# Optimization experiments

Hardware: AMD Instinct MI355X
Metric: run time of the kernel (lower is better)

The kernel has to match this reference:

```python
import jax, jax.numpy as jnp
import numpy as np

B = 65536
IN_F = 1024
OUT_F = 1024


def setup_inputs() -> dict:
    key = jax.random.key(0)
    k1, k2 = jax.random.split(key)
    x = jax.random.normal(k1, (B, IN_F), dtype=jnp.float32)
    # init matches torch: normal(0, sqrt(2/(in+out)))
    std = np.sqrt(2.0 / (IN_F + OUT_F)).astype(np.float32)
    weight = jax.random.normal(k2, (OUT_F, IN_F), dtype=jnp.float32) * std
    bias = jnp.zeros((OUT_F,), dtype=jnp.float32)
    return {"x": x, "weight": weight, "bias": bias}


def reference(x, weight, bias):
    # Deterministic binarization: sign(w) in {-1, 0, +1} (sign(0)=0, same as torch)
    w_bin = jnp.sign(weight)
    # [B, in] @ [in, out] + [out]
    return jnp.matmul(x, w_bin.T) + bias[None, :]
```

## Files before the change

### kernel.cpp

```cpp
#include <hip/hip_runtime.h>


typedef __bf16 bf16x8 __attribute__((ext_vector_type(8)));
typedef __bf16 bf16x4 __attribute__((ext_vector_type(4)));
typedef float  f32x4  __attribute__((ext_vector_type(4)));

constexpr int Mdim = 65536, Ndim = 1024, Kdim = 1024;
constexpr int BM = 256, BN = 256, BK = 64;
constexpr int NKT = Kdim / BK;
constexpr int NWG = (Mdim / BM) * (Ndim / BN);

typedef const __attribute__((address_space(1))) char ga_char;
typedef __attribute__((address_space(3))) char lds_char;
__device__ __forceinline__ void gload16(const void* g, void* l) {
    __builtin_amdgcn_global_load_lds((ga_char*)g, (lds_char*)l, 16, 0, 0);
}
__device__ __forceinline__ f32x4 mfma16(bf16x8 a, bf16x8 b, f32x4 c) {
    return __builtin_amdgcn_mfma_f32_16x16x32_bf16(a, b, c, 0, 0, 0);
}
#define BARRIER()    asm volatile("s_barrier" ::: "memory")
#define WAIT_VM0()   asm volatile("s_waitcnt vmcnt(0)" ::: "memory")
#define WAIT_LGKM0() asm volatile("s_waitcnt lgkmcnt(0)" ::: "memory")

__global__ __launch_bounds__(256)
void wprep_kernel(const float* __restrict__ W, __bf16* __restrict__ WS) {
    const int id = blockIdx.x * 256 + threadIdx.x;
    const int c  = id & 7;
    const int kt = (id >> 3) & 15;
    const int n  = id >> 7;
    const float* src = W + (size_t)n * Kdim + kt * 64 + c * 8;
    f32x4 a = *(const f32x4*)src;
    f32x4 b = *(const f32x4*)(src + 4);
    bf16x8 o;
#pragma unroll
    for (int e = 0; e < 4; ++e) {
        o[e]     = (__bf16)(float)((a[e] > 0.f) - (a[e] < 0.f));
        o[e + 4] = (__bf16)(float)((b[e] > 0.f) - (b[e] < 0.f));
    }
    const int row  = n & 255;
    const int colb = n >> 8;
    __bf16* dst = WS + (size_t)(colb * 16 + kt) * 16384
                + row * 64 + ((c ^ (row & 7)) * 8);
    *(bf16x8*)dst = o;
}

__global__ __launch_bounds__(512, 2)
void binlin256(const float* __restrict__ X, const __bf16* __restrict__ WS,
               const float* __restrict__ bias, float* __restrict__ out)
{
    __shared__ __align__(16) __bf16 Al[2][BM * BK];
    __shared__ __align__(16) __bf16 Bl[2][BN * BK];

    const int swz  = (blockIdx.x & 7) * (NWG / 8) + (blockIdx.x >> 3);
    const int colb = swz & 3;
    const int rowb = swz >> 2;
    const int row0 = rowb * BM;

    const int tid  = threadIdx.x;
    const int lane = tid & 63;
    const int wid  = tid >> 6;
    const int wr   = wid >> 2;
    const int wcn  = wid & 3;
    const int fr   = lane & 15;
    const int hq   = lane >> 4;

    const int a_r = tid >> 2;
    const int a_c = (tid & 3) * 16;
    const float* Xb = X + (size_t)(row0 + a_r) * Kdim + a_c;

    const __bf16* WSb = WS + (size_t)colb * 16 * 16384;

    f32x4 rA0[4], rA1[4];

    auto GLA0 = [&](int kt) {
        const float* p = Xb + kt * 64;
#pragma unroll
        for (int q = 0; q < 4; ++q) rA0[q] = *(const f32x4*)(p + q * 4);
    };
    auto GLA1 = [&](int kt) {
        const float* p = Xb + (size_t)128 * Kdim + kt * 64;
#pragma unroll
        for (int q = 0; q < 4; ++q) rA1[q] = *(const f32x4*)(p + q * 4);
    };
    auto DSWA = [&](int buf, int h, f32x4* r) {
        const int row = h * 128 + a_r;
#pragma unroll
        for (int w = 0; w < 2; ++w) {
            bf16x8 v;
#pragma unroll
            for (int e = 0; e < 4; ++e) {
                v[e]     = (__bf16)r[w * 2][e];
                v[e + 4] = (__bf16)r[w * 2 + 1][e];
            }
            const int c    = (a_c >> 3) + w;
            const int byte = row * 128 + ((c ^ (row & 7)) << 4);
            *(bf16x8*)((char*)&Al[buf][0] + byte) = v;
        }
    };
    auto GLB = [&](int buf, int kt) {
        const __bf16* s0 = WSb + (size_t)kt * 16384 + wid * 2048 + lane * 8;
#pragma unroll
        for (int i = 0; i < 4; ++i)
            gload16(s0 + i * 512, &Bl[buf][wid * 2048 + i * 512]);
    };

    auto lda = [&](int buf, int i, int ks) -> bf16x8 {
        const int row  = wr * 128 + i * 16 + fr;
        const int byte = row * 128 + (((ks * 4 + hq) ^ (row & 7)) << 4);
        return *(const bf16x8*)((const char*)&Al[buf][0] + byte);
    };
    auto ldb = [&](int buf, int j, int ks) -> bf16x8 {
        const int row  = wcn * 64 + j * 16 + fr;
        const int byte = row * 128 + (((ks * 4 + hq) ^ (row & 7)) << 4);
        return *(const bf16x8*)((const char*)&Bl[buf][0] + byte);
    };

    f32x4 acc[8][4] = {};

    GLA0(0); GLA1(0); GLB(0, 0);
    DSWA(0, 0, rA0); DSWA(0, 1, rA1);
    __syncthreads();

    int cur = 0;
    for (int kt = 0; kt < NKT; ++kt) {
        const int nxt = cur ^ 1;
        const bool pre = (kt + 1 < NKT);
        bf16x8 a[4], b0[4], b1[4];

        if (pre) GLA0(kt + 1);
#pragma unroll
        for (int j = 0; j < 4; ++j) b0[j] = ldb(cur, j, 0);
#pragma unroll
        for (int i = 0; i < 4; ++i) a[i] = lda(cur, i, 0);
        __builtin_amdgcn_s_setprio(1);
#pragma unroll
        for (int i = 0; i < 4; ++i)
#pragma unroll
            for (int j = 0; j < 4; ++j)
                acc[i][j] = mfma16(a[i], b0[j], acc[i][j]);
        __builtin_amdgcn_s_setprio(0);
        BARRIER();

        if (pre) GLA1(kt + 1);
#pragma unroll
        for (int i = 0; i < 4; ++i) a[i] = lda(cur, i + 4, 0);
        __builtin_amdgcn_s_setprio(1);
#pragma unroll
        for (int i = 0; i < 4; ++i)
#pragma unroll
            for (int j = 0; j < 4; ++j)
                acc[i + 4][j] = mfma16(a[i], b0[j], acc[i + 4][j]);
        __builtin_amdgcn_s_setprio(0);
        BARRIER();

        if (pre) { GLB(nxt, kt + 1); DSWA(nxt, 0, rA0); }
#pragma unroll
        for (int j = 0; j < 4; ++j) b1[j] = ldb(cur, j, 1);
#pragma unroll
        for (int i = 0; i < 4; ++i) a[i] = lda(cur, i, 1);
        __builtin_amdgcn_s_setprio(1);
#pragma unroll
        for (int i = 0; i < 4; ++i)
#pragma unroll
            for (int j = 0; j < 4; ++j)
                acc[i][j] = mfma16(a[i], b1[j], acc[i][j]);
        __builtin_amdgcn_s_setprio(0);
        BARRIER();

        if (pre) DSWA(nxt, 1, rA1);
#pragma unroll
        for (int i = 0; i < 4; ++i) a[i] = lda(cur, i + 4, 1);
        __builtin_amdgcn_s_setprio(1);
#pragma unroll
        for (int i = 0; i < 4; ++i)
#pragma unroll
            for (int j = 0; j < 4; ++j)
                acc[i + 4][j] = mfma16(a[i], b1[j], acc[i + 4][j]);
        __builtin_amdgcn_s_setprio(0);
        if (pre) {
            WAIT_LGKM0();
            WAIT_VM0();
        }
        BARRIER();
        cur = nxt;
    }

    const int orow = row0 + wr * 128 + hq * 4;
    const int ocol = colb * 256 + wcn * 64 + fr;
#pragma unroll
    for (int j = 0; j < 4; ++j) {
        const float bv = bias[ocol + j * 16];
#pragma unroll
        for (int i = 0; i < 8; ++i)
#pragma unroll
            for (int r = 0; r < 4; ++r)
                out[(size_t)(orow + i * 16 + r) * Ndim + (ocol + j * 16)] =
                    acc[i][j][r] + bv;
    }
}

__global__ __launch_bounds__(256)
void binlin_fallback(const float* __restrict__ X, const float* __restrict__ Wf,
                     const float* __restrict__ bias, float* __restrict__ out)
{
    __shared__ __align__(16) __bf16 Al[2][128][32];
    __shared__ __align__(16) __bf16 Bl[2][128][32];
    constexpr int NT = Kdim / 32;
    const int swz  = (blockIdx.x & 7) * (4096 / 8) + (blockIdx.x >> 3);
    const int colb = swz & 7, rowb = swz >> 3;
    const int row0 = rowb * 128, col0 = colb * 128;
    const int tid = threadIdx.x, lane = tid & 63, wid = tid >> 6;
    const int wr = wid >> 1, wc = wid & 1;
    const int sr = tid >> 2, sc = (tid & 3) * 8;
    const float* Xb = X + (size_t)row0 * Kdim;
    const float* Wb = Wf + (size_t)col0 * Kdim;
    f32x4 ra[2][2], rb[2][2];
    auto GL = [&](int k0) {
#pragma unroll
        for (int p = 0; p < 2; ++p) {
            const float* sa = Xb + (size_t)(p * 64 + sr) * Kdim + k0 + sc;
            ra[p][0] = *(const f32x4*)sa; ra[p][1] = *(const f32x4*)(sa + 4);
            const float* sb = Wb + (size_t)(p * 64 + sr) * Kdim + k0 + sc;
            rb[p][0] = *(const f32x4*)sb; rb[p][1] = *(const f32x4*)(sb + 4);
        }
    };
    auto DSW = [&](int buf) {
#pragma unroll
        for (int p = 0; p < 2; ++p) {
            bf16x8 va, vb;
#pragma unroll
            for (int e = 0; e < 4; ++e) {
                va[e] = (__bf16)ra[p][0][e]; va[e + 4] = (__bf16)ra[p][1][e];
                float a = rb[p][0][e], b = rb[p][1][e];
                vb[e] = (__bf16)(float)((a > 0.f) - (a < 0.f));
                vb[e + 4] = (__bf16)(float)((b > 0.f) - (b < 0.f));
            }
            *(bf16x8*)&Al[buf][p * 64 + sr][sc] = va;
            *(bf16x8*)&Bl[buf][p * 64 + sr][sc] = vb;
        }
    };
    f32x4 acc[4][4] = {};
    const int fr = lane & 15, ks = (lane >> 4) * 8;
    auto COMP = [&](int buf) {
        bf16x8 af[4], bf[4];
#pragma unroll
        for (int i = 0; i < 4; ++i) af[i] = *(const bf16x8*)&Al[buf][wr * 64 + fr + i * 16][ks];
#pragma unroll
        for (int j = 0; j < 4; ++j) bf[j] = *(const bf16x8*)&Bl[buf][wc * 64 + fr + j * 16][ks];
#pragma unroll
        for (int i = 0; i < 4; ++i)
#pragma unroll
            for (int j = 0; j < 4; ++j)
                acc[i][j] = mfma16(af[i], bf[j], acc[i][j]);
    };
    GL(0); DSW(0); __syncthreads();
    int cur = 0;
    for (int t = 0; t < NT; ++t) {
        if (t + 1 < NT) GL((t + 1) * 32);
        COMP(cur);
        if (t + 1 < NT) { DSW(cur ^ 1); __syncthreads(); cur ^= 1; }
    }
    const int orow = row0 + wr * 64 + (lane >> 4) * 4;
    const int ocol = col0 + wc * 64 + fr;
#pragma unroll
    for (int j = 0; j < 4; ++j) {
        const float bv = bias[ocol + j * 16];
#pragma unroll
        for (int i = 0; i < 4; ++i)
#pragma unroll
            for (int r = 0; r < 4; ++r)
                out[(size_t)(orow + i * 16 + r) * Ndim + (ocol + j * 16)] = acc[i][j][r] + bv;
    }
}

extern "C" void kernel_launch(void* const* d_in, const int* in_sizes, int n_in,
                              void* d_out, int out_size, void* d_ws, size_t ws_size,
                              hipStream_t stream) {
    const float* x  = (const float*)d_in[0];
    const float* w  = (const float*)d_in[1];
    const float* b  = (const float*)d_in[2];
    float* out      = (float*)d_out;

    constexpr size_t WS_BYTES = (size_t)Ndim * Kdim * sizeof(__bf16);

    if (ws_size >= WS_BYTES) {
        __bf16* ws = (__bf16*)d_ws;
        wprep_kernel<<<dim3(512), dim3(256), 0, stream>>>(w, ws);
        binlin256<<<dim3(NWG), dim3(512), 0, stream>>>(x, ws, b, out);
    } else {
        binlin_fallback<<<dim3(4096), dim3(256), 0, stream>>>(x, w, b, out);
    }
}
```

Before: 243.1 us.

## Use MFMA-fragment-ordered LDS layout and deeper A-prefetch pipeline

Reorders the pre-binarized weight image and the LDS tiles so that each MFMA fragment is a contiguous 512-element block. Per-lane loads become simple linear addresses with no XOR swizzle. The main loop is rescheduled so that X global loads run two K-tiles ahead. B global-to-LDS loads and the A stores into LDS for the next tile are split across the four phases, with partial vmcnt waits instead of a full drain. The risk is LDS bank conflicts in the new contiguous layout and correctness of the partial wait counts.

```diff
diff --git a/kernel.cpp b/kernel.cpp
--- a/kernel.cpp
+++ b/kernel.cpp
@@ -2,7 +2,6 @@
 
 
 typedef __bf16 bf16x8 __attribute__((ext_vector_type(8)));
-typedef __bf16 bf16x4 __attribute__((ext_vector_type(4)));
 typedef float  f32x4  __attribute__((ext_vector_type(4)));
 
 constexpr int Mdim = 65536, Ndim = 1024, Kdim = 1024;
@@ -18,17 +17,20 @@
 __device__ __forceinline__ f32x4 mfma16(bf16x8 a, bf16x8 b, f32x4 c) {
     return __builtin_amdgcn_mfma_f32_16x16x32_bf16(a, b, c, 0, 0, 0);
 }
-#define BARRIER()    asm volatile("s_barrier" ::: "memory")
-#define WAIT_VM0()   asm volatile("s_waitcnt vmcnt(0)" ::: "memory")
-#define WAIT_LGKM0() asm volatile("s_waitcnt lgkmcnt(0)" ::: "memory")
 
 __global__ __launch_bounds__(256)
-void wprep_kernel(const float* __restrict__ W, __bf16* __restrict__ WS) {
-    const int id = blockIdx.x * 256 + threadIdx.x;
-    const int c  = id & 7;
-    const int kt = (id >> 3) & 15;
-    const int n  = id >> 7;
-    const float* src = W + (size_t)n * Kdim + kt * 64 + c * 8;
+void wprep_kernel(const float* __restrict__ W, __bf16* __restrict__ WB) {
+    const int id   = blockIdx.x * 256 + threadIdx.x;
+    const int lane = id & 63;
+    const int g    = id >> 6;
+    const int nb   = g & 7;
+    const int ks   = (g >> 3) & 1;
+    const int half = (g >> 4) & 1;
+    const int kt   = (g >> 5) & 15;
+    const int colb = g >> 9;
+    const int row  = colb * 256 + half * 128 + nb * 16 + (lane & 15);
+    const int col  = kt * 64 + ks * 32 + (lane >> 4) * 8;
+    const float* src = W + (size_t)row * Kdim + col;
     f32x4 a = *(const f32x4*)src;
     f32x4 b = *(const f32x4*)(src + 4);
     bf16x8 o;
@@ -37,19 +39,15 @@
         o[e]     = (__bf16)(float)((a[e] > 0.f) - (a[e] < 0.f));
         o[e + 4] = (__bf16)(float)((b[e] > 0.f) - (b[e] < 0.f));
     }
-    const int row  = n & 255;
-    const int colb = n >> 8;
-    __bf16* dst = WS + (size_t)(colb * 16 + kt) * 16384
-                + row * 64 + ((c ^ (row & 7)) * 8);
-    *(bf16x8*)dst = o;
+    *(bf16x8*)(WB + (size_t)id * 8) = o;
 }
 
 __global__ __launch_bounds__(512, 2)
-void binlin256(const float* __restrict__ X, const __bf16* __restrict__ WS,
+void binlin_t8(const float* __restrict__ X, const __bf16* __restrict__ WB,
                const float* __restrict__ bias, float* __restrict__ out)
 {
-    __shared__ __align__(16) __bf16 Al[2][BM * BK];
-    __shared__ __align__(16) __bf16 Bl[2][BN * BK];
+    __shared__ __align__(16) __bf16 Al[2][16384];
+    __shared__ __align__(16) __bf16 Bl[2][16384];
 
     const int swz  = (blockIdx.x & 7) * (NWG / 8) + (blockIdx.x >> 3);
     const int colb = swz & 3;
@@ -64,126 +62,138 @@
     const int fr   = lane & 15;
     const int hq   = lane >> 4;
 
-    const int a_r = tid >> 2;
-    const int a_c = (tid & 3) * 16;
-    const float* Xb = X + (size_t)(row0 + a_r) * Kdim + a_c;
-
-    const __bf16* WSb = WS + (size_t)colb * 16 * 16384;
+    const int rl   = tid >> 2;
+    const int fc   = tid & 3;
+    const int mb_s = rl >> 4, rr_s = rl & 15;
+    const int s_s  = fc >> 1,  kh_s = fc & 1;
+    const float* Xr0 = X + (size_t)(row0 + rl) * Kdim + fc * 16;
+    const float* Xr1 = Xr0 + (size_t)128 * Kdim;
+
+    const __bf16* WBb = WB + (size_t)colb * 262144;
 
     f32x4 rA0[4], rA1[4];
 
     auto GLA0 = [&](int kt) {
-        const float* p = Xb + kt * 64;
+        const float* p = Xr0 + kt * BK;
 #pragma unroll
         for (int q = 0; q < 4; ++q) rA0[q] = *(const f32x4*)(p + q * 4);
     };
     auto GLA1 = [&](int kt) {
-        const float* p = Xb + (size_t)128 * Kdim + kt * 64;
+        const float* p = Xr1 + kt * BK;
 #pragma unroll
         for (int q = 0; q < 4; ++q) rA1[q] = *(const f32x4*)(p + q * 4);
     };
-    auto DSWA = [&](int buf, int h, f32x4* r) {
-        const int row = h * 128 + a_r;
-#pragma unroll
-        for (int w = 0; w < 2; ++w) {
+    auto DSW = [&](int buf, int h) {
+        const f32x4* r = h ? rA1 : rA0;
+        const int base = h * 8192 + s_s * 4096 + mb_s * 512;
+#pragma unroll
+        for (int jj = 0; jj < 2; ++jj) {
             bf16x8 v;
 #pragma unroll
             for (int e = 0; e < 4; ++e) {
-                v[e]     = (__bf16)r[w * 2][e];
-                v[e + 4] = (__bf16)r[w * 2 + 1][e];
+                v[e]     = (__bf16)r[jj * 2][e];
+                v[e + 4] = (__bf16)r[jj * 2 + 1][e];
             }
-            const int c    = (a_c >> 3) + w;
-            const int byte = row * 128 + ((c ^ (row & 7)) << 4);
-            *(bf16x8*)((char*)&Al[buf][0] + byte) = v;
+            *(bf16x8*)&Al[buf][base + ((kh_s * 2 + jj) * 16 + rr_s) * 8] = v;
         }
     };
-    auto GLB = [&](int buf, int kt) {
-        const __bf16* s0 = WSb + (size_t)kt * 16384 + wid * 2048 + lane * 8;
-#pragma unroll
-        for (int i = 0; i < 4; ++i)
-            gload16(s0 + i * 512, &Bl[buf][wid * 2048 + i * 512]);
+    auto GLB = [&](int buf, int kt, int half) {
+        const __bf16* img = WBb + (size_t)(kt * 2 + half) * 8192;
+#pragma unroll
+        for (int r = 0; r < 2; ++r) {
+            const int chunk = r * 8 + wid;
+            gload16(img + chunk * 512 + lane * 8,
+                    &Bl[buf][half * 8192 + chunk * 512]);
+        }
     };
 
     auto lda = [&](int buf, int i, int ks) -> bf16x8 {
-        const int row  = wr * 128 + i * 16 + fr;
-        const int byte = row * 128 + (((ks * 4 + hq) ^ (row & 7)) << 4);
-        return *(const bf16x8*)((const char*)&Al[buf][0] + byte);
+        return *(const bf16x8*)&Al[buf][wr * 8192 + ks * 4096 + i * 512 + lane * 8];
     };
     auto ldb = [&](int buf, int j, int ks) -> bf16x8 {
-        const int row  = wcn * 64 + j * 16 + fr;
-        const int byte = row * 128 + (((ks * 4 + hq) ^ (row & 7)) << 4);
-        return *(const bf16x8*)((const char*)&Bl[buf][0] + byte);
-    };
+        const int nbg = wcn * 4 + j;
+        return *(const bf16x8*)&Bl[buf][(nbg >> 3) * 8192 + (ks * 8 + (nbg & 7)) * 512 + lane * 8];
+    };
+
+#define PHASE_SYNC() do { __builtin_amdgcn_s_barrier();                        \
+    asm volatile("s_waitcnt lgkmcnt(0)" ::: "memory");                         \
+    __builtin_amdgcn_sched_barrier(0); } while (0)
 
     f32x4 acc[8][4] = {};
-
-    GLA0(0); GLA1(0); GLB(0, 0);
-    DSWA(0, 0, rA0); DSWA(0, 1, rA1);
+    bf16x8 af[4], bf[4];
+
+    GLB(0, 0, 0); GLB(0, 0, 1);
+    GLA0(0); GLA1(0);
+    DSW(0, 0); DSW(0, 1);
+    GLA0(1); GLA1(1);
     __syncthreads();
 
-    int cur = 0;
-    for (int kt = 0; kt < NKT; ++kt) {
-        const int nxt = cur ^ 1;
-        const bool pre = (kt + 1 < NKT);
-        bf16x8 a[4], b0[4], b1[4];
-
-        if (pre) GLA0(kt + 1);
-#pragma unroll
-        for (int j = 0; j < 4; ++j) b0[j] = ldb(cur, j, 0);
-#pragma unroll
-        for (int i = 0; i < 4; ++i) a[i] = lda(cur, i, 0);
+    for (int t = 0; t < NKT; ++t) {
+        const int c  = t & 1;
+        const int n  = c ^ 1;
+        const int tS = (t + 1 < NKT) ? t + 1 : NKT - 1;
+        const int tA = (t + 2 < NKT) ? t + 2 : NKT - 1;
+
+#pragma unroll
+        for (int j = 0; j < 4; ++j) bf[j] = ldb(c, j, 0);
+#pragma unroll
+        for (int i = 0; i < 4; ++i) af[i] = lda(c, i, 0);
+        GLB(n, tS, 0);
+        DSW(n, 0);
+        PHASE_SYNC();
         __builtin_amdgcn_s_setprio(1);
 #pragma unroll
         for (int i = 0; i < 4; ++i)
 #pragma unroll
             for (int j = 0; j < 4; ++j)
-                acc[i][j] = mfma16(a[i], b0[j], acc[i][j]);
+                acc[i][j] = mfma16(af[i], bf[j], acc[i][j]);
         __builtin_amdgcn_s_setprio(0);
-        BARRIER();
-
-        if (pre) GLA1(kt + 1);
-#pragma unroll
-        for (int i = 0; i < 4; ++i) a[i] = lda(cur, i + 4, 0);
+        __builtin_amdgcn_s_barrier();
+
+#pragma unroll
+        for (int i = 0; i < 4; ++i) af[i] = lda(c, 4 + i, 0);
+        GLB(n, tS, 1);
+        PHASE_SYNC();
         __builtin_amdgcn_s_setprio(1);
 #pragma unroll
         for (int i = 0; i < 4; ++i)
 #pragma unroll
             for (int j = 0; j < 4; ++j)
-                acc[i + 4][j] = mfma16(a[i], b0[j], acc[i + 4][j]);
+                acc[4 + i][j] = mfma16(af[i], bf[j], acc[4 + i][j]);
         __builtin_amdgcn_s_setprio(0);
-        BARRIER();
-
-        if (pre) { GLB(nxt, kt + 1); DSWA(nxt, 0, rA0); }
-#pragma unroll
-        for (int j = 0; j < 4; ++j) b1[j] = ldb(cur, j, 1);
-#pragma unroll
-        for (int i = 0; i < 4; ++i) a[i] = lda(cur, i, 1);
+        __builtin_amdgcn_s_barrier();
+
+#pragma unroll
+        for (int j = 0; j < 4; ++j) bf[j] = ldb(c, j, 1);
+#pragma unroll
+        for (int i = 0; i < 4; ++i) af[i] = lda(c, i, 1);
+        GLA0(tA);
+        DSW(n, 1);
+        PHASE_SYNC();
         __builtin_amdgcn_s_setprio(1);
 #pragma unroll
         for (int i = 0; i < 4; ++i)
 #pragma unroll
             for (int j = 0; j < 4; ++j)
-                acc[i][j] = mfma16(a[i], b1[j], acc[i][j]);
+                acc[i][j] = mfma16(af[i], bf[j], acc[i][j]);
         __builtin_amdgcn_s_setprio(0);
-        BARRIER();
-
-        if (pre) DSWA(nxt, 1, rA1);
-#pragma unroll
-        for (int i = 0; i < 4; ++i) a[i] = lda(cur, i + 4, 1);
+        __builtin_amdgcn_s_barrier();
+
+#pragma unroll
+        for (int i = 0; i < 4; ++i) af[i] = lda(c, 4 + i, 1);
+        GLA1(tA);
+        PHASE_SYNC();
         __builtin_amdgcn_s_setprio(1);
 #pragma unroll
         for (int i = 0; i < 4; ++i)
 #pragma unroll
             for (int j = 0; j < 4; ++j)
-                acc[i + 4][j] = mfma16(a[i], b1[j], acc[i + 4][j]);
+                acc[4 + i][j] = mfma16(af[i], bf[j], acc[4 + i][j]);
         __builtin_amdgcn_s_setprio(0);
-        if (pre) {
-            WAIT_LGKM0();
-            WAIT_VM0();
-        }
-        BARRIER();
-        cur = nxt;
-    }
+        asm volatile("s_waitcnt vmcnt(8)" ::: "memory");
+        __builtin_amdgcn_s_barrier();
+    }
+#undef PHASE_SYNC
 
     const int orow = row0 + wr * 128 + hq * 4;
     const int ocol = colb * 256 + wcn * 64 + fr;
@@ -281,12 +291,12 @@
     const float* b  = (const float*)d_in[2];
     float* out      = (float*)d_out;
 
-    constexpr size_t WS_BYTES = (size_t)Ndim * Kdim * sizeof(__bf16);
-
-    if (ws_size >= WS_BYTES) {
-        __bf16* ws = (__bf16*)d_ws;
-        wprep_kernel<<<dim3(512), dim3(256), 0, stream>>>(w, ws);
-        binlin256<<<dim3(NWG), dim3(512), 0, stream>>>(x, ws, b, out);
+    constexpr size_t WB_BYTES = (size_t)Ndim * Kdim * sizeof(__bf16);
+
+    if (ws_size >= WB_BYTES) {
+        __bf16* wb = (__bf16*)d_ws;
+        wprep_kernel<<<dim3(512), dim3(256), 0, stream>>>(w, wb);
+        binlin_t8<<<dim3(NWG), dim3(512), 0, stream>>>(x, wb, b, out);
     } else {
         binlin_fallback<<<dim3(4096), dim3(256), 0, stream>>>(x, w, b, out);
     }
```

Result: slower. 275.7 us (+13.4%).
